# Performance work log

Hardware: AMD Instinct MI355X
Metric: run time of the kernel (lower is better)

Reference implementation:

```python
import jax, jax.numpy as jnp
import numpy as np

B = 16          # number of graphs in the batch (fixed for segment ops)
PTS = 4096      # points per graph
N = B * PTS
C = 256         # input feature channels
EPS = 1e-16     # PyG knn_interpolate eps


def setup_inputs() -> dict:
    key = jax.random.key(0)
    ks = jax.random.split(key, 12)
    x = jax.random.normal(ks[0], (N, C), dtype=jnp.float32)
    pos = jax.random.normal(ks[1], (N, 3), dtype=jnp.float32)
    x_skip = jax.random.normal(ks[2], (N, C), dtype=jnp.float32)
    pos_skip = jax.random.normal(ks[3], (N, 3), dtype=jnp.float32)
    # sorted segment ids, every graph populated
    batch = jnp.repeat(jnp.arange(B, dtype=jnp.int32), PTS)
    batch_skip = jnp.repeat(jnp.arange(B, dtype=jnp.int32), PTS)
    # MLP([C+3, 256, 512, 1024]) parameters (Linear + ReLU per layer)
    s = 0.02
    W1 = jax.random.normal(ks[4], (C + 3, 256), dtype=jnp.float32) * s
    b1 = jnp.zeros((256,), dtype=jnp.float32)
    W2 = jax.random.normal(ks[5], (256, 512), dtype=jnp.float32) * s
    b2 = jnp.zeros((512,), dtype=jnp.float32)
    W3 = jax.random.normal(ks[6], (512, 1024), dtype=jnp.float32) * s
    b3 = jnp.zeros((1024,), dtype=jnp.float32)
    return {"x": x, "pos": pos, "batch": batch, "x_skip": x_skip,
            "pos_skip": pos_skip, "batch_skip": batch_skip,
            "W1": W1, "b1": b1, "W2": W2, "b2": b2, "W3": W3, "b3": b3}


def reference(x, pos, batch, x_skip, pos_skip, batch_skip, W1, b1, W2, b2, W3, b3):
    # nn(cat([x, pos], dim=1)): 3-layer MLP with ReLU
    h = jnp.concatenate([x, pos], axis=1)            # [N, C+3]
    h = jax.nn.relu(h @ W1 + b1)                     # [N, 256]
    h = jax.nn.relu(h @ W2 + b2)                     # [N, 512]
    h = jax.nn.relu(h @ W3 + b3)                     # [N, 1024]
    # global_max_pool over each graph
    pooled = jax.ops.segment_max(h, batch, num_segments=B)  # [B, 1024]
    # knn_interpolate(pooled, origin-per-graph, pos_skip, k=3):
    # each graph contributes exactly ONE source point (the origin), so the
    # single in-batch neighbor gets inverse-distance weight that normalizes
    # to 1; written explicitly to mirror the PyG weighting math.
    d2 = jnp.sum(pos_skip * pos_skip, axis=1, keepdims=True)  # [Ns, 1] dist^2 to origin
    w = 1.0 / (d2 + EPS)
    gathered = pooled[batch_skip]                    # [Ns, 1024]
    interp = (w * gathered) / w                      # weights cancel -> gathered
    # cat with skip features
    out = jnp.concatenate([interp, x_skip], axis=1)  # [Ns, 1024 + C]
    return out
```

## Files before the change

kernel.cpp:

```cpp
#include <hip/hip_runtime.h>
#include <hip/hip_bf16.h>


typedef __attribute__((ext_vector_type(8))) short bf16x8;
typedef __attribute__((ext_vector_type(4))) float f32x4;

#define GLD_LDS16(src, dst) __builtin_amdgcn_global_load_lds( \
    (const __attribute__((address_space(1))) unsigned int*)(src), \
    (__attribute__((address_space(3))) unsigned int*)(dst), 16, 0, 0)

__device__ __forceinline__ unsigned short f2bf(float f) {
  unsigned int u = __float_as_uint(f);
  unsigned int r = (u + 0x7FFFu + ((u >> 16) & 1u)) >> 16;
  return (unsigned short)r;
}
__device__ __forceinline__ float bf2f(unsigned short h) {
  return __uint_as_float(((unsigned int)h) << 16);
}

__global__ void pack_a1(const float* __restrict__ x, const float* __restrict__ pos,
                        unsigned short* __restrict__ ah, unsigned short* __restrict__ al) {
  const int n = blockIdx.x;
  const int c = threadIdx.x;
  float v = 0.f;
  if (c < 256)      v = x[(size_t)n * 256 + c];
  else if (c < 259) v = pos[(size_t)n * 3 + (c - 256)];
  unsigned short hi = f2bf(v);
  ah[(size_t)n * 320 + c] = hi;
  al[(size_t)n * 320 + c] = f2bf(v - bf2f(hi));
}

__global__ void pack_w(const float* __restrict__ w, unsigned short* __restrict__ wh,
                       unsigned short* __restrict__ wl, int K, int Nout) {
  const int no = blockIdx.x;
  const int k = threadIdx.x;
  const int KP = blockDim.x;
  float v = (k < K) ? w[(size_t)k * Nout + no] : 0.f;
  unsigned short hi = f2bf(v);
  wh[(size_t)no * KP + k] = hi;
  wl[(size_t)no * KP + k] = f2bf(v - bf2f(hi));
}

__global__ void zero_pool(unsigned int* __restrict__ p) {
  p[blockIdx.x * 1024 + threadIdx.x] = 0u;
}

template<int KP, int NOUT, int MODE>
__global__ __launch_bounds__(256, 2)
void gemm_split(const unsigned short* __restrict__ gAh, const unsigned short* __restrict__ gAl,
                const unsigned short* __restrict__ gBh, const unsigned short* __restrict__ gBl,
                const float* __restrict__ bias,
                unsigned short* __restrict__ Ch, unsigned short* __restrict__ Cl,
                unsigned int* __restrict__ pooled, const int* __restrict__ batch) {
  constexpr int BM = 128, BN = 128, BK = 64;
  constexpr int NB = NOUT / BN;
  __shared__ unsigned short lds[4 * BM * BK];

  const int nwg = gridDim.x;
  const int bid = (blockIdx.x % 8) * (nwg / 8) + blockIdx.x / 8;
  const int bm = bid / NB, bn = bid % NB;
  const int r0 = bm * BM, c0 = bn * BN;
  const int tid = threadIdx.x;
  const int lane = tid & 63, wid = tid >> 6;
  const int wm = wid >> 1, wc = wid & 1;
  const int al15 = lane & 15, l4 = lane >> 4;
  const int swz = lane & 7, lr = lane >> 3;

  f32x4 acc[4][4] = {};

  const unsigned short* plane = (wid == 0) ? gAh : (wid == 1) ? gAl : (wid == 2) ? gBh : gBl;
  const int rb = (wid < 2) ? r0 : c0;
  unsigned short* sbase = lds + wid * (BM * BK);
  const unsigned short* gsrc0 = plane + (size_t)(rb + lr) * KP + ((swz ^ lr) << 3);
  unsigned short* ldst0 = sbase + lane * 8;

  for (int kt = 0; kt < KP / BK; ++kt) {
    {
      const unsigned short* s = gsrc0 + kt * BK;
      unsigned short* d = ldst0;
      #pragma unroll
      for (int t = 0; t < 16; ++t) {
        GLD_LDS16(s, d);
        s += 8 * KP;
        d += 512;
      }
    }
    __syncthreads();

    const unsigned short* sA_h = lds;
    const unsigned short* sA_l = lds + BM * BK;
    const unsigned short* sB_h = lds + 2 * BM * BK;
    const unsigned short* sB_l = lds + 3 * BM * BK;

    #pragma unroll
    for (int ks = 0; ks < BK / 32; ++ks) {
      bf16x8 fah[4], fal[4], fbh[4], fbl[4];
      const int kc = ks * 4 + l4;
      #pragma unroll
      for (int i = 0; i < 4; ++i) {
        const int arow = wm * 64 + i * 16 + al15;
        const int aoff = arow * BK + ((kc ^ swz) << 3);
        fah[i] = *(const bf16x8*)(sA_h + aoff);
        fal[i] = *(const bf16x8*)(sA_l + aoff);
        const int brow = wc * 64 + i * 16 + al15;
        const int boff = brow * BK + ((kc ^ swz) << 3);
        fbh[i] = *(const bf16x8*)(sB_h + boff);
        fbl[i] = *(const bf16x8*)(sB_l + boff);
      }
      #pragma unroll
      for (int i = 0; i < 4; ++i)
        #pragma unroll
        for (int j = 0; j < 4; ++j) {
          acc[i][j] = __builtin_amdgcn_mfma_f32_16x16x32_bf16(fah[i], fbh[j], acc[i][j], 0, 0, 0);
          acc[i][j] = __builtin_amdgcn_mfma_f32_16x16x32_bf16(fah[i], fbl[j], acc[i][j], 0, 0, 0);
          acc[i][j] = __builtin_amdgcn_mfma_f32_16x16x32_bf16(fal[i], fbh[j], acc[i][j], 0, 0, 0);
        }
    }
    __syncthreads();
  }

  if (MODE == 0) {
    #pragma unroll
    for (int j = 0; j < 4; ++j) {
      const int col = c0 + wc * 64 + j * 16 + al15;
      const float bz = bias[col];
      #pragma unroll
      for (int i = 0; i < 4; ++i) {
        const int row0 = r0 + wm * 64 + i * 16 + l4 * 4;
        #pragma unroll
        for (int r = 0; r < 4; ++r) {
          float v = fmaxf(acc[i][j][r] + bz, 0.f);
          unsigned short hi = f2bf(v);
          Ch[(size_t)(row0 + r) * NOUT + col] = hi;
          Cl[(size_t)(row0 + r) * NOUT + col] = f2bf(v - bf2f(hi));
        }
      }
    }
  } else {
    const int g = batch[r0];
    float* pb = (float*)lds;
    #pragma unroll
    for (int j = 0; j < 4; ++j) {
      const int col128 = wc * 64 + j * 16 + al15;
      const float bz = bias[c0 + col128];
      float cm = 0.f;
      #pragma unroll
      for (int i = 0; i < 4; ++i)
        #pragma unroll
        for (int r = 0; r < 4; ++r)
          cm = fmaxf(cm, acc[i][j][r] + bz);
      cm = fmaxf(cm, __shfl_xor(cm, 16));
      cm = fmaxf(cm, __shfl_xor(cm, 32));
      if (l4 == 0) pb[wm * 128 + col128] = cm;
    }
    __syncthreads();
    if (tid < 128) {
      float m = fmaxf(pb[tid], pb[128 + tid]);
      atomicMax(pooled + (size_t)g * 1024 + c0 + tid, __float_as_uint(m));
    }
  }
}

__global__ void write_out(const float* __restrict__ pooled, const float* __restrict__ x_skip,
                          const int* __restrict__ batch_skip, float* __restrict__ out,
                          int N) {
  const int t = threadIdx.x;
  for (int n = blockIdx.x; n < N; n += gridDim.x) {
    const int g = batch_skip[n];
    const float4* ps = (const float4*)(pooled + (size_t)g * 1024);
    float4* o = (float4*)(out + (size_t)n * 1280);
    o[t] = ps[t];
    if (t < 64) {
      const float4* xs = (const float4*)(x_skip + (size_t)n * 256);
      o[256 + t] = xs[t];
    }
  }
}

extern "C" void kernel_launch(void* const* d_in, const int* in_sizes, int n_in,
                              void* d_out, int out_size, void* d_ws, size_t ws_size,
                              hipStream_t stream) {
  const float* x        = (const float*)d_in[0];
  const float* pos      = (const float*)d_in[1];
  const int*   batch    = (const int*)d_in[2];
  const float* x_skip   = (const float*)d_in[3];
  const int*   batch_sk = (const int*)d_in[5];
  const float* W1 = (const float*)d_in[6];
  const float* b1 = (const float*)d_in[7];
  const float* W2 = (const float*)d_in[8];
  const float* b2 = (const float*)d_in[9];
  const float* W3 = (const float*)d_in[10];
  const float* b3 = (const float*)d_in[11];
  float* out = (float*)d_out;

  char* ws = (char*)d_ws;
  unsigned short* a1h = (unsigned short*)(ws);
  unsigned short* a1l = (unsigned short*)(ws + 41943040);
  unsigned short* h2h = (unsigned short*)(ws);
  unsigned short* h2l = (unsigned short*)(ws + 67108864);
  size_t off = 134217728;
  unsigned short* h1h = (unsigned short*)(ws + off); off += 33554432;
  unsigned short* h1l = (unsigned short*)(ws + off); off += 33554432;
  unsigned short* w1h = (unsigned short*)(ws + off); off += 163840;
  unsigned short* w1l = (unsigned short*)(ws + off); off += 163840;
  unsigned short* w2h = (unsigned short*)(ws + off); off += 262144;
  unsigned short* w2l = (unsigned short*)(ws + off); off += 262144;
  unsigned short* w3h = (unsigned short*)(ws + off); off += 1048576;
  unsigned short* w3l = (unsigned short*)(ws + off); off += 1048576;
  unsigned int*  pooled = (unsigned int*)(ws + off);

  hipLaunchKernelGGL(pack_w, dim3(256),  dim3(320), 0, stream, W1, w1h, w1l, 259, 256);
  hipLaunchKernelGGL(pack_w, dim3(512),  dim3(256), 0, stream, W2, w2h, w2l, 256, 512);
  hipLaunchKernelGGL(pack_w, dim3(1024), dim3(512), 0, stream, W3, w3h, w3l, 512, 1024);
  hipLaunchKernelGGL(pack_a1, dim3(65536), dim3(320), 0, stream, x, pos, a1h, a1l);
  hipLaunchKernelGGL(zero_pool, dim3(16), dim3(1024), 0, stream, pooled);

  hipLaunchKernelGGL((gemm_split<320, 256, 0>), dim3(512 * 2), dim3(256), 0, stream,
                     a1h, a1l, w1h, w1l, b1, h1h, h1l,
                     (unsigned int*)nullptr, (const int*)nullptr);
  hipLaunchKernelGGL((gemm_split<256, 512, 0>), dim3(512 * 4), dim3(256), 0, stream,
                     h1h, h1l, w2h, w2l, b2, h2h, h2l,
                     (unsigned int*)nullptr, (const int*)nullptr);
  hipLaunchKernelGGL((gemm_split<512, 1024, 1>), dim3(512 * 8), dim3(256), 0, stream,
                     h2h, h2l, w3h, w3l, b3,
                     (unsigned short*)nullptr, (unsigned short*)nullptr, pooled, batch);

  hipLaunchKernelGGL(write_out, dim3(2048), dim3(256), 0, stream,
                     (const float*)pooled, x_skip, batch_sk, out, 65536);
}
```

Measured before the change: 785.3 us.

## Switch GEMMs to 32x32x16 MFMA, vectorize pack_a1, widen write_out grid

Replaces the 16x16x32 bf16 MFMA tiling with 32x32x16 MFMA (2x2 tiles of 16-float accumulators per wave), recomputing LDS fragment addressing with a row-based swizzle and remapping the epilogue and max-pool reduction to the new output layout. The larger instruction halves the number of fragment loads per FLOP and is meant to raise matrix-core throughput in the three split-bf16 GEMMs. pack_a1 becomes a grid-stride kernel that handles float4 per thread and writes ushort4, and write_out gets twice as many blocks. Risks include LDS bank conflicts under the new swizzle and higher register pressure from 64 accumulators per wave.

```diff
diff --git a/kernel.cpp b/kernel.cpp
--- a/kernel.cpp
+++ b/kernel.cpp
@@ -3,7 +3,7 @@
 
 
 typedef __attribute__((ext_vector_type(8))) short bf16x8;
-typedef __attribute__((ext_vector_type(4))) float f32x4;
+typedef __attribute__((ext_vector_type(16))) float f32x16;
 
 #define GLD_LDS16(src, dst) __builtin_amdgcn_global_load_lds( \
     (const __attribute__((address_space(1))) unsigned int*)(src), \
@@ -20,14 +20,30 @@
 
 __global__ void pack_a1(const float* __restrict__ x, const float* __restrict__ pos,
                         unsigned short* __restrict__ ah, unsigned short* __restrict__ al) {
-  const int n = blockIdx.x;
-  const int c = threadIdx.x;
-  float v = 0.f;
-  if (c < 256)      v = x[(size_t)n * 256 + c];
-  else if (c < 259) v = pos[(size_t)n * 3 + (c - 256)];
-  unsigned short hi = f2bf(v);
-  ah[(size_t)n * 320 + c] = hi;
-  al[(size_t)n * 320 + c] = f2bf(v - bf2f(hi));
+  const int total = 65536 * 80;
+  for (int idx = blockIdx.x * blockDim.x + threadIdx.x; idx < total;
+       idx += gridDim.x * blockDim.x) {
+    const int n = idx / 80;
+    const int q = idx - n * 80;
+    float4 v;
+    if (q < 64) {
+      v = ((const float4*)x)[(size_t)n * 64 + q];
+    } else if (q == 64) {
+      v.x = pos[(size_t)n * 3 + 0];
+      v.y = pos[(size_t)n * 3 + 1];
+      v.z = pos[(size_t)n * 3 + 2];
+      v.w = 0.f;
+    } else {
+      v.x = v.y = v.z = v.w = 0.f;
+    }
+    ushort4 h, l;
+    h.x = f2bf(v.x); l.x = f2bf(v.x - bf2f(h.x));
+    h.y = f2bf(v.y); l.y = f2bf(v.y - bf2f(h.y));
+    h.z = f2bf(v.z); l.z = f2bf(v.z - bf2f(h.z));
+    h.w = f2bf(v.w); l.w = f2bf(v.w - bf2f(h.w));
+    *(ushort4*)(ah + (size_t)n * 320 + q * 4) = h;
+    *(ushort4*)(al + (size_t)n * 320 + q * 4) = l;
+  }
 }
 
 __global__ void pack_w(const float* __restrict__ w, unsigned short* __restrict__ wh,
@@ -63,10 +79,10 @@
   const int tid = threadIdx.x;
   const int lane = tid & 63, wid = tid >> 6;
   const int wm = wid >> 1, wc = wid & 1;
-  const int al15 = lane & 15, l4 = lane >> 4;
+  const int al31 = lane & 31, l5 = lane >> 5;
   const int swz = lane & 7, lr = lane >> 3;
 
-  f32x4 acc[4][4] = {};
+  f32x16 acc[2][2] = {};
 
   const unsigned short* plane = (wid == 0) ? gAh : (wid == 1) ? gAl : (wid == 2) ? gBh : gBl;
   const int rb = (wid < 2) ? r0 : c0;
@@ -93,27 +109,27 @@
     const unsigned short* sB_l = lds + 3 * BM * BK;
 
     #pragma unroll
-    for (int ks = 0; ks < BK / 32; ++ks) {
-      bf16x8 fah[4], fal[4], fbh[4], fbl[4];
-      const int kc = ks * 4 + l4;
-      #pragma unroll
-      for (int i = 0; i < 4; ++i) {
-        const int arow = wm * 64 + i * 16 + al15;
-        const int aoff = arow * BK + ((kc ^ swz) << 3);
+    for (int ks = 0; ks < BK / 16; ++ks) {
+      bf16x8 fah[2], fal[2], fbh[2], fbl[2];
+      const int cb = ks * 2 + l5;
+      #pragma unroll
+      for (int i = 0; i < 2; ++i) {
+        const int arow = wm * 64 + i * 32 + al31;
+        const int aoff = arow * BK + ((cb ^ (arow & 7)) << 3);
         fah[i] = *(const bf16x8*)(sA_h + aoff);
         fal[i] = *(const bf16x8*)(sA_l + aoff);
-        const int brow = wc * 64 + i * 16 + al15;
-        const int boff = brow * BK + ((kc ^ swz) << 3);
+        const int brow = wc * 64 + i * 32 + al31;
+        const int boff = brow * BK + ((cb ^ (brow & 7)) << 3);
         fbh[i] = *(const bf16x8*)(sB_h + boff);
         fbl[i] = *(const bf16x8*)(sB_l + boff);
       }
       #pragma unroll
-      for (int i = 0; i < 4; ++i)
+      for (int i = 0; i < 2; ++i)
         #pragma unroll
-        for (int j = 0; j < 4; ++j) {
-          acc[i][j] = __builtin_amdgcn_mfma_f32_16x16x32_bf16(fah[i], fbh[j], acc[i][j], 0, 0, 0);
-          acc[i][j] = __builtin_amdgcn_mfma_f32_16x16x32_bf16(fah[i], fbl[j], acc[i][j], 0, 0, 0);
-          acc[i][j] = __builtin_amdgcn_mfma_f32_16x16x32_bf16(fal[i], fbh[j], acc[i][j], 0, 0, 0);
+        for (int j = 0; j < 2; ++j) {
+          acc[i][j] = __builtin_amdgcn_mfma_f32_32x32x16_bf16(fah[i], fbh[j], acc[i][j], 0, 0, 0);
+          acc[i][j] = __builtin_amdgcn_mfma_f32_32x32x16_bf16(fah[i], fbl[j], acc[i][j], 0, 0, 0);
+          acc[i][j] = __builtin_amdgcn_mfma_f32_32x32x16_bf16(fal[i], fbh[j], acc[i][j], 0, 0, 0);
         }
     }
     __syncthreads();
@@ -121,18 +137,19 @@
 
   if (MODE == 0) {
     #pragma unroll
-    for (int j = 0; j < 4; ++j) {
-      const int col = c0 + wc * 64 + j * 16 + al15;
-      const float bz = bias[col];
-      #pragma unroll
-      for (int i = 0; i < 4; ++i) {
-        const int row0 = r0 + wm * 64 + i * 16 + l4 * 4;
+    for (int i = 0; i < 2; ++i) {
+      const int rbase = r0 + wm * 64 + i * 32 + 4 * l5;
+      #pragma unroll
+      for (int j = 0; j < 2; ++j) {
+        const int col = c0 + wc * 64 + j * 32 + al31;
+        const float bz = bias[col];
         #pragma unroll
-        for (int r = 0; r < 4; ++r) {
+        for (int r = 0; r < 16; ++r) {
+          const int row = rbase + (r & 3) + 8 * (r >> 2);
           float v = fmaxf(acc[i][j][r] + bz, 0.f);
           unsigned short hi = f2bf(v);
-          Ch[(size_t)(row0 + r) * NOUT + col] = hi;
-          Cl[(size_t)(row0 + r) * NOUT + col] = f2bf(v - bf2f(hi));
+          Ch[(size_t)row * NOUT + col] = hi;
+          Cl[(size_t)row * NOUT + col] = f2bf(v - bf2f(hi));
         }
       }
     }
@@ -140,18 +157,17 @@
     const int g = batch[r0];
     float* pb = (float*)lds;
     #pragma unroll
-    for (int j = 0; j < 4; ++j) {
-      const int col128 = wc * 64 + j * 16 + al15;
-      const float bz = bias[c0 + col128];
+    for (int j = 0; j < 2; ++j) {
+      const int colw = wc * 64 + j * 32 + al31;
+      const float bz = bias[c0 + colw];
       float cm = 0.f;
       #pragma unroll
-      for (int i = 0; i < 4; ++i)
+      for (int i = 0; i < 2; ++i)
         #pragma unroll
-        for (int r = 0; r < 4; ++r)
+        for (int r = 0; r < 16; ++r)
           cm = fmaxf(cm, acc[i][j][r] + bz);
-      cm = fmaxf(cm, __shfl_xor(cm, 16));
       cm = fmaxf(cm, __shfl_xor(cm, 32));
-      if (l4 == 0) pb[wm * 128 + col128] = cm;
+      if (l5 == 0) pb[wm * 128 + colw] = cm;
     }
     __syncthreads();
     if (tid < 128) {
@@ -212,7 +228,7 @@
   hipLaunchKernelGGL(pack_w, dim3(256),  dim3(320), 0, stream, W1, w1h, w1l, 259, 256);
   hipLaunchKernelGGL(pack_w, dim3(512),  dim3(256), 0, stream, W2, w2h, w2l, 256, 512);
   hipLaunchKernelGGL(pack_w, dim3(1024), dim3(512), 0, stream, W3, w3h, w3l, 512, 1024);
-  hipLaunchKernelGGL(pack_a1, dim3(65536), dim3(320), 0, stream, x, pos, a1h, a1l);
+  hipLaunchKernelGGL(pack_a1, dim3(2048), dim3(256), 0, stream, x, pos, a1h, a1l);
   hipLaunchKernelGGL(zero_pool, dim3(16), dim3(1024), 0, stream, pooled);
 
   hipLaunchKernelGGL((gemm_split<320, 256, 0>), dim3(512 * 2), dim3(256), 0, stream,
@@ -225,6 +241,6 @@
                      h2h, h2l, w3h, w3l, b3,
                      (unsigned short*)nullptr, (unsigned short*)nullptr, pooled, batch);
 
-  hipLaunchKernelGGL(write_out, dim3(2048), dim3(256), 0, stream,
+  hipLaunchKernelGGL(write_out, dim3(4096), dim3(256), 0, stream,
                      (const float*)pooled, x_skip, batch_sk, out, 65536);
 }
```

Result: no change. 771.1 us (-1.8%).
